# Kernel tuning notes

Measured on AMD Instinct MI355X. Metric: run time of the kernel, lower is better.

## Reference

```python
import jax, jax.numpy as jnp
import numpy as np

EPS = 1e-12

def _l2norm(x):
    n = jnp.sqrt(jnp.sum(x * x, axis=-1, keepdims=True))
    return x / jnp.maximum(n, EPS)

def setup_inputs() -> dict:
    key = jax.random.key(0)
    k1, k2 = jax.random.split(key)
    B, S, H = 32, 256, 768
    return {
        "query_embs": jax.random.normal(k1, (B, S, H), dtype=jnp.float32),
        "key_embs": jax.random.normal(k2, (B, S, H), dtype=jnp.float32),
        "q_mask": jnp.ones((B, S), dtype=jnp.float32),
        "k_mask": jnp.ones((B, S), dtype=jnp.float32),
        "alpha_raw": jnp.asarray(1.0, dtype=jnp.float32),
        "logit_scale": jnp.asarray(0.0, dtype=jnp.float32),  # log(1.0)
    }

def reference(query_embs, key_embs, q_mask, k_mask, alpha_raw, logit_scale):
    # query_embs, key_embs: (B, S, H); masks: (B, S)
    S = query_embs.shape[1]
    q = _l2norm(query_embs)
    k = _l2norm(key_embs)
    # all-pairs token similarity: (B, B, S, T)
    sim = jnp.einsum('ish,jth->ijst', q, k)
    # distance-decay weighting (do_distance=True, exp_decay=True)
    alpha = jax.nn.softplus(alpha_raw)
    pos = jnp.arange(S, dtype=jnp.float32)
    dist = jnp.abs(pos[:, None] - pos[None, :])  # (S, S)
    sim = sim * jnp.exp(-alpha * dist)
    # validity mask: (B, B, S, T)
    valid = (q_mask[:, None, :, None] * k_mask[None, :, None, :]) > 0
    scale = jnp.exp(logit_scale)
    neg_inf = jnp.float32(-jnp.inf)
    logits = jnp.where(valid, scale * sim, neg_inf)
    all_inf = jnp.all(logits == neg_inf, axis=-1, keepdims=True)
    safe_logits = jnp.where(all_inf, 0.0, logits)
    p = jax.nn.softmax(safe_logits, axis=-1)
    p = jnp.where(all_inf, 0.0, p)
    # softmax-weighted key aggregation: (B, B, S, H)
    agg = jnp.einsum('ijst,jth->ijsh', p, k)
    # per-token cosine score, masked mean over query tokens
    scores = jnp.einsum('ish,ijsh->ijs', q, agg) * q_mask[:, None, :]
    denom = jnp.clip(jnp.sum(q_mask, axis=-1, keepdims=True), 1.0, None)
    return jnp.sum(scores, axis=-1) / denom  # (B, B)
```

## Files before the change

kernel.cpp:

```cpp
#include <hip/hip_runtime.h>
#include <cmath>

#define BB 32
#define SS 256
#define HH 768

typedef __attribute__((ext_vector_type(8))) short bfrag8;
typedef __attribute__((ext_vector_type(4))) float accf4;

__device__ __forceinline__ unsigned short f2bf(float x) {
    unsigned int b = __float_as_uint(x);
    return (unsigned short)((b + 0x7FFFu + ((b >> 16) & 1u)) >> 16);
}

__device__ __forceinline__ float bf2f(unsigned short u) {
    unsigned int b = ((unsigned int)u) << 16;
    return __uint_as_float(b);
}


__global__ __launch_bounds__(256)
void normcvt_kernel(const float* __restrict__ Q, const float* __restrict__ K,
                    unsigned short* __restrict__ qws, unsigned short* __restrict__ kws) {
    const int wave = threadIdx.x >> 6, lane = threadIdx.x & 63;
    const bool isQ = blockIdx.x < 2048;
    const int rr = (blockIdx.x * 4 + wave) & 8191;
    const float4* src4 = isQ ? (const float4*)(Q + (size_t)rr * HH)
                             : (const float4*)(K + (size_t)rr * HH);
    float4 vv[3]; float s = 0.f;
#pragma unroll
    for (int c = 0; c < 3; ++c) {
        vv[c] = src4[lane + 64 * c];
        s += vv[c].x * vv[c].x + vv[c].y * vv[c].y + vv[c].z * vv[c].z + vv[c].w * vv[c].w;
    }
#pragma unroll
    for (int off = 1; off < 64; off <<= 1) s += __shfl_xor(s, off);
    float inv = 1.f / fmaxf(sqrtf(s), 1e-12f);

    const int b = rr >> 8, srow = rr & 255;
    unsigned short* dst = isQ ? qws : kws;
    const int fp8 = (lane & 7) * 4;
#pragma unroll
    for (int c = 0; c < 3; ++c) {
        int kc = (lane >> 3) + 8 * c;
        ushort4 o;
        o.x = f2bf(vv[c].x * inv); o.y = f2bf(vv[c].y * inv);
        o.z = f2bf(vv[c].z * inv); o.w = f2bf(vv[c].w * inv);
        *(ushort4*)(dst + (((size_t)b * 24 + kc) * 256 + srow) * 32 + fp8) = o;
    }
}

__global__ __launch_bounds__(256)
void ksum_kernel(const unsigned short* __restrict__ kws, const float* __restrict__ kmask,
                 unsigned short* __restrict__ ksumB) {
    __shared__ float red[8][32];
    const int j = blockIdx.x / 24, kc = blockIdx.x - j * 24;
    const int e = threadIdx.x & 31, tg = threadIdx.x >> 5;
    const unsigned short* base = kws + ((size_t)(j * 24 + kc)) * 8192;
    const float* km = kmask + j * SS;
    float s = 0.f;
    for (int t = tg; t < 256; t += 8) {
        if (km[t] > 0.f) s += bf2f(base[t * 32 + e]);
    }
    red[tg][e] = s;
    __syncthreads();
    if (tg == 0) {
        float tot = 0.f;
#pragma unroll
        for (int g = 0; g < 8; ++g) tot += red[g][e];
        ksumB[(size_t)(j * 24 + kc) * 32 + e] = f2bf(tot);
    }
}

__global__ __launch_bounds__(256, 3)
void mfma_kernel(const unsigned short* __restrict__ qws, const unsigned short* __restrict__ kws,
                 const float* __restrict__ qmask, const float* __restrict__ kmask,
                 const float* __restrict__ araw_p, const float* __restrict__ lscale_p,
                 const unsigned short* __restrict__ ksumB, float* __restrict__ out) {
    __shared__ short lKsum[768];
    __shared__ float sKm[256];
    __shared__ float wtab[13];
    __shared__ float sRed[4][2];
    __shared__ float sPart[4];
    __shared__ float sKcnt, sQden;

    const int tid = threadIdx.x;
    const int lane = tid & 63, w = tid >> 6;
    const int quad = lane >> 4, col = lane & 15;
    const int i = blockIdx.x >> 5, j = blockIdx.x & 31;

    const float alpha = log1pf(__expf(araw_p[0]));
    const float scale = __expf(lscale_p[0]);

    float aq = qmask[i * SS + tid];
    float km = kmask[j * SS + tid];
    sKm[tid] = km;
    float c = (km > 0.f) ? 1.f : 0.f;
#pragma unroll
    for (int off = 1; off < 64; off <<= 1) { aq += __shfl_xor(aq, off); c += __shfl_xor(c, off); }
    if (lane == 0) { sRed[w][0] = aq; sRed[w][1] = c; }
    if (tid < 13) wtab[tid] = __expf(-alpha * (float)tid);
    if (tid < 192) ((ushort4*)lKsum)[tid] = ((const ushort4*)(ksumB + (size_t)j * HH))[tid];
    __syncthreads();
    if (tid == 0) {
        sQden = fmaxf(sRed[0][0] + sRed[1][0] + sRed[2][0] + sRed[3][0], 1.f);
        sKcnt = sRed[0][1] + sRed[1][1] + sRed[2][1] + sRed[3][1];
    }
    __syncthreads();

    accf4 acc[4][3];
    accf4 accB[4];
#pragma unroll
    for (int a = 0; a < 4; ++a) {
        accB[a] = (accf4)0.f;
#pragma unroll
        for (int b = 0; b < 3; ++b) acc[a][b] = (accf4)0.f;
    }

    const unsigned short* qp0 = qws + (size_t)i * 24 * 8192 + (size_t)(4 * w) * 512
                                    + col * 32 + quad * 8;
    const unsigned short* kp0 = kws + (size_t)j * 24 * 8192 + col * 32 + quad * 8;

    for (int kc = 0; kc < 24; ++kc) {
        const unsigned short* qp = qp0 + (size_t)kc * 8192;
        const unsigned short* kp = kp0 + (size_t)kc * 8192;
        bfrag8 af[4];
#pragma unroll
        for (int sbl = 0; sbl < 4; ++sbl)
            af[sbl] = *(const bfrag8*)(qp + sbl * 512);
        bfrag8 bfr[6];
#pragma unroll
        for (int u = 0; u < 6; ++u) {
            int tb = 4 * w - 1 + u;
            if (tb >= 0 && tb <= 15)
                bfr[u] = *(const bfrag8*)(kp + tb * 512);
        }
        const bfrag8 kfrag = *(const bfrag8*)(lKsum + kc * 32 + quad * 8);
#pragma unroll
        for (int sbl = 0; sbl < 4; ++sbl) {
            accB[sbl] = __builtin_amdgcn_mfma_f32_16x16x32_bf16(af[sbl], kfrag, accB[sbl], 0, 0, 0);
#pragma unroll
            for (int dtb = 0; dtb < 3; ++dtb) {
                int tb = 4 * w + sbl - 1 + dtb;
                if (tb >= 0 && tb <= 15)
                    acc[sbl][dtb] = __builtin_amdgcn_mfma_f32_16x16x32_bf16(
                        af[sbl], bfr[sbl + dtb], acc[sbl][dtb], 0, 0, 0);
            }
        }
    }

    const float kcnt = sKcnt;
    float part = 0.f;
#pragma unroll
    for (int sbl = 0; sbl < 4; ++sbl) {
        const int sbase = (4 * w + sbl) * 16 + quad * 4;
        float ns[4] = {0.f, 0.f, 0.f, 0.f}, ds[4] = {0.f, 0.f, 0.f, 0.f};
#pragma unroll
        for (int dtb = 0; dtb < 3; ++dtb) {
            int tb = 4 * w + sbl - 1 + dtb;
            if (tb < 0 || tb > 15) continue;
            int t = tb * 16 + col;
            float kmv = sKm[t];
#pragma unroll
            for (int reg = 0; reg < 4; ++reg) {
                int st = sbase + reg;
                int d = t - st;
                bool ok = (d >= -11) && (d <= 12) && (kmv > 0.f);
                int idx = d < 0 ? -d : d;
                idx = ok ? idx : 0;
                float raw = acc[sbl][dtb][reg];
                float e = ok ? expm1f(scale * raw * wtab[idx]) : 0.f;
                ns[reg] = fmaf(e, raw, ns[reg]);
                ds[reg] += e;
            }
        }
#pragma unroll
        for (int off = 1; off < 16; off <<= 1) {
#pragma unroll
            for (int reg = 0; reg < 4; ++reg) {
                ns[reg] += __shfl_xor(ns[reg], off);
                ds[reg] += __shfl_xor(ds[reg], off);
            }
        }
        if (col == 0) {
#pragma unroll
            for (int reg = 0; reg < 4; ++reg) {
                int st = sbase + reg;
                float qm = qmask[i * SS + st];
                float bse = accB[sbl][reg];
                float dtot = ds[reg] + kcnt;
                float v = (qm > 0.f && kcnt > 0.f) ? qm * (ns[reg] + bse) / dtot : 0.f;
                part += v;
            }
        }
    }
    part += __shfl_xor(part, 16);
    part += __shfl_xor(part, 32);
    if (lane == 0) sPart[w] = part;
    __syncthreads();
    if (tid == 0) out[i * BB + j] = (sPart[0] + sPart[1] + sPart[2] + sPart[3]) / sQden;
}


extern "C" void kernel_launch(void* const* d_in, const int* in_sizes, int n_in,
                              void* d_out, int out_size, void* d_ws, size_t ws_size,
                              hipStream_t stream) {
    const float* Q      = (const float*)d_in[0];
    const float* K      = (const float*)d_in[1];
    const float* qmask  = (const float*)d_in[2];
    const float* kmask  = (const float*)d_in[3];
    const float* araw   = (const float*)d_in[4];
    const float* lscale = (const float*)d_in[5];
    float* outp = (float*)d_out;

    unsigned short* ksumB = (unsigned short*)d_ws;
    unsigned short* qws = ksumB + 24576;
    unsigned short* kws = qws + 6291456;

    normcvt_kernel<<<4096, 256, 0, stream>>>(Q, K, qws, kws);
    ksum_kernel<<<768, 256, 0, stream>>>(kws, kmask, ksumB);
    mfma_kernel<<<1024, 256, 0, stream>>>(qws, kws, qmask, kmask, araw, lscale, ksumB, outp);
}
```

Measured before the change: 175.8 us.

## Stage K tiles into LDS with double-buffered async global_load_lds and swizzle

The MFMA kernel now copies each 256x32 bf16 K chunk into shared memory using async global-to-LDS loads. It uses two buffers so the next chunk loads while the current one is computed. Before, every wave read its overlapping K fragments straight from global memory. The K workspace layout is XOR-swizzled in normcvt so the LDS fragment reads avoid bank conflicts, and ksum_kernel is rewritten to read that swizzled layout with vectorised loads. Occupancy is raised to 4 blocks per SM, which adds about 33KB of LDS per block and extra barriers per iteration.

Result: slower. 272.5 us (+55.0%).

```diff
diff --git a/kernel.cpp b/kernel.cpp
--- a/kernel.cpp
+++ b/kernel.cpp
@@ -16,6 +16,11 @@
 __device__ __forceinline__ float bf2f(unsigned short u) {
     unsigned int b = ((unsigned int)u) << 16;
     return __uint_as_float(b);
+}
+
+__device__ __forceinline__ void gload16(const void* g, void* l) {
+    __builtin_amdgcn_global_load_lds((const __attribute__((address_space(1))) void*)g,
+                                     (__attribute__((address_space(3))) void*)l, 16, 0, 0);
 }
 
 
@@ -39,7 +44,9 @@
 
     const int b = rr >> 8, srow = rr & 255;
     unsigned short* dst = isQ ? qws : kws;
-    const int fp8 = (lane & 7) * 4;
+    const int e = (lane & 7) * 4;
+    const int fp8 = isQ ? e
+                        : ((((e >> 3) ^ ((srow >> 1) & 3)) << 3) + (e & 7));
 #pragma unroll
     for (int c = 0; c < 3; ++c) {
         int kc = (lane >> 3) + 8 * c;
@@ -53,30 +60,46 @@
 __global__ __launch_bounds__(256)
 void ksum_kernel(const unsigned short* __restrict__ kws, const float* __restrict__ kmask,
                  unsigned short* __restrict__ ksumB) {
-    __shared__ float red[8][32];
+    __shared__ float red[4][8][4];
     const int j = blockIdx.x / 24, kc = blockIdx.x - j * 24;
-    const int e = threadIdx.x & 31, tg = threadIdx.x >> 5;
+    const int lane = threadIdx.x & 63, wv = threadIdx.x >> 6;
+    const int tg = threadIdx.x >> 3;
+    const int ec = threadIdx.x & 7;
     const unsigned short* base = kws + ((size_t)(j * 24 + kc)) * 8192;
     const float* km = kmask + j * SS;
-    float s = 0.f;
-    for (int t = tg; t < 256; t += 8) {
-        if (km[t] > 0.f) s += bf2f(base[t * 32 + e]);
-    }
-    red[tg][e] = s;
+    const int f = ec >> 1, off4 = (ec & 1) * 4;
+    float s0 = 0.f, s1 = 0.f, s2 = 0.f, s3 = 0.f;
+    for (int t = tg; t < 256; t += 32) {
+        if (km[t] > 0.f) {
+            int pos = ((f ^ ((t >> 1) & 3)) << 3) + off4;
+            ushort4 v = *(const ushort4*)(base + t * 32 + pos);
+            s0 += bf2f(v.x); s1 += bf2f(v.y); s2 += bf2f(v.z); s3 += bf2f(v.w);
+        }
+    }
+#pragma unroll
+    for (int off = 8; off < 64; off <<= 1) {
+        s0 += __shfl_xor(s0, off); s1 += __shfl_xor(s1, off);
+        s2 += __shfl_xor(s2, off); s3 += __shfl_xor(s3, off);
+    }
+    if ((lane >> 3) == 0) {
+        red[wv][ec][0] = s0; red[wv][ec][1] = s1; red[wv][ec][2] = s2; red[wv][ec][3] = s3;
+    }
     __syncthreads();
-    if (tg == 0) {
-        float tot = 0.f;
-#pragma unroll
-        for (int g = 0; g < 8; ++g) tot += red[g][e];
+    if (threadIdx.x < 32) {
+        int e = threadIdx.x;
+        float tot = red[0][e >> 2][e & 3] + red[1][e >> 2][e & 3]
+                  + red[2][e >> 2][e & 3] + red[3][e >> 2][e & 3];
         ksumB[(size_t)(j * 24 + kc) * 32 + e] = f2bf(tot);
     }
 }
 
-__global__ __launch_bounds__(256, 3)
+__global__ __launch_bounds__(256, 4)
 void mfma_kernel(const unsigned short* __restrict__ qws, const unsigned short* __restrict__ kws,
                  const float* __restrict__ qmask, const float* __restrict__ kmask,
                  const float* __restrict__ araw_p, const float* __restrict__ lscale_p,
                  const unsigned short* __restrict__ ksumB, float* __restrict__ out) {
+    __shared__ short lk0[8192];
+    __shared__ short lk1[8192];
     __shared__ short lKsum[768];
     __shared__ float sKm[256];
     __shared__ float wtab[13];
@@ -101,53 +124,71 @@
     if (lane == 0) { sRed[w][0] = aq; sRed[w][1] = c; }
     if (tid < 13) wtab[tid] = __expf(-alpha * (float)tid);
     if (tid < 192) ((ushort4*)lKsum)[tid] = ((const ushort4*)(ksumB + (size_t)j * HH))[tid];
+
+    accf4 acc[4][3];
+    accf4 accB[4];
+#pragma unroll
+    for (int a = 0; a < 4; ++a) {
+        accB[a] = (accf4)0.f;
+#pragma unroll
+        for (int b = 0; b < 3; ++b) acc[a][b] = (accf4)0.f;
+    }
+
+    const unsigned short* qp0 = qws + (size_t)i * 24 * 8192 + (size_t)(4 * w) * 512
+                                    + col * 32 + quad * 8;
+    const unsigned short* ksrc = kws + (size_t)j * 24 * 8192 + (size_t)w * 2048 + lane * 8;
+    const int perm8 = ((quad ^ ((col >> 1) & 3)) << 3);
+
+#define STAGEK(BUF, KCN) { \
+    unsigned short* _d = (unsigned short*)(BUF) + w * 2048; \
+    const unsigned short* _s = ksrc + (size_t)(KCN) * 8192; \
+    gload16(_s, _d); gload16(_s + 512, _d + 512); \
+    gload16(_s + 1024, _d + 1024); gload16(_s + 1536, _d + 1536); }
+
+#define COMPUTE(BUF, KC) { \
+    const unsigned short* _qp = qp0 + (size_t)(KC) * 8192; \
+    bfrag8 af[4]; \
+    af[0] = *(const bfrag8*)(_qp); \
+    af[1] = *(const bfrag8*)(_qp + 512); \
+    af[2] = *(const bfrag8*)(_qp + 1024); \
+    af[3] = *(const bfrag8*)(_qp + 1536); \
+    bfrag8 bfr[6]; \
+    _Pragma("unroll") \
+    for (int u = 0; u < 6; ++u) { \
+        int tb = 4 * w - 1 + u; \
+        if (tb >= 0 && tb <= 15) \
+            bfr[u] = *(const bfrag8*)((const short*)(BUF) + (size_t)(tb * 16 + col) * 32 + perm8); \
+    } \
+    const bfrag8 kfrag = *(const bfrag8*)(lKsum + (KC) * 32 + quad * 8); \
+    _Pragma("unroll") \
+    for (int sbl = 0; sbl < 4; ++sbl) { \
+        accB[sbl] = __builtin_amdgcn_mfma_f32_16x16x32_bf16(af[sbl], kfrag, accB[sbl], 0, 0, 0); \
+        _Pragma("unroll") \
+        for (int dtb = 0; dtb < 3; ++dtb) { \
+            int tb = 4 * w + sbl - 1 + dtb; \
+            if (tb >= 0 && tb <= 15) \
+                acc[sbl][dtb] = __builtin_amdgcn_mfma_f32_16x16x32_bf16( \
+                    af[sbl], bfr[sbl + dtb], acc[sbl][dtb], 0, 0, 0); \
+        } \
+    } }
+
+    STAGEK(lk0, 0);
     __syncthreads();
     if (tid == 0) {
         sQden = fmaxf(sRed[0][0] + sRed[1][0] + sRed[2][0] + sRed[3][0], 1.f);
         sKcnt = sRed[0][1] + sRed[1][1] + sRed[2][1] + sRed[3][1];
     }
-    __syncthreads();
-
-    accf4 acc[4][3];
-    accf4 accB[4];
-#pragma unroll
-    for (int a = 0; a < 4; ++a) {
-        accB[a] = (accf4)0.f;
-#pragma unroll
-        for (int b = 0; b < 3; ++b) acc[a][b] = (accf4)0.f;
-    }
-
-    const unsigned short* qp0 = qws + (size_t)i * 24 * 8192 + (size_t)(4 * w) * 512
-                                    + col * 32 + quad * 8;
-    const unsigned short* kp0 = kws + (size_t)j * 24 * 8192 + col * 32 + quad * 8;
-
-    for (int kc = 0; kc < 24; ++kc) {
-        const unsigned short* qp = qp0 + (size_t)kc * 8192;
-        const unsigned short* kp = kp0 + (size_t)kc * 8192;
-        bfrag8 af[4];
-#pragma unroll
-        for (int sbl = 0; sbl < 4; ++sbl)
-            af[sbl] = *(const bfrag8*)(qp + sbl * 512);
-        bfrag8 bfr[6];
-#pragma unroll
-        for (int u = 0; u < 6; ++u) {
-            int tb = 4 * w - 1 + u;
-            if (tb >= 0 && tb <= 15)
-                bfr[u] = *(const bfrag8*)(kp + tb * 512);
-        }
-        const bfrag8 kfrag = *(const bfrag8*)(lKsum + kc * 32 + quad * 8);
-#pragma unroll
-        for (int sbl = 0; sbl < 4; ++sbl) {
-            accB[sbl] = __builtin_amdgcn_mfma_f32_16x16x32_bf16(af[sbl], kfrag, accB[sbl], 0, 0, 0);
-#pragma unroll
-            for (int dtb = 0; dtb < 3; ++dtb) {
-                int tb = 4 * w + sbl - 1 + dtb;
-                if (tb >= 0 && tb <= 15)
-                    acc[sbl][dtb] = __builtin_amdgcn_mfma_f32_16x16x32_bf16(
-                        af[sbl], bfr[sbl + dtb], acc[sbl][dtb], 0, 0, 0);
-            }
-        }
-    }
+
+    for (int kc = 0; kc < 24; kc += 2) {
+        STAGEK(lk1, kc + 1);
+        COMPUTE(lk0, kc);
+        __syncthreads();
+        if (kc + 2 < 24) STAGEK(lk0, kc + 2);
+        COMPUTE(lk1, kc + 1);
+        __syncthreads();
+    }
+#undef STAGEK
+#undef COMPUTE
 
     const float kcnt = sKcnt;
     float part = 0.f;
```

## Stage K chunks into swizzled LDS via global_load_lds in MFMA kernel

Applied to the files above, without the earlier changes.

The MFMA kernel now copies each 256x32 K chunk into shared memory with direct global-to-LDS loads, then reads B fragments from LDS instead of global memory. Each K row is XOR-swizzled in the workspace layout to avoid LDS bank conflicts, and ksum is rewritten to read the swizzled layout with vectorized loads and shuffle reductions. Occupancy hint goes from 3 to 4 blocks. The goal is to stop each wave re-fetching overlapping K tiles from global memory; the cost is two block barriers per K step and 16KB more LDS per block.

New measurement: 153.8 us. -12.5%, faster.

```diff
diff --git a/kernel.cpp b/kernel.cpp
--- a/kernel.cpp
+++ b/kernel.cpp
@@ -14,8 +14,12 @@
 }
 
 __device__ __forceinline__ float bf2f(unsigned short u) {
-    unsigned int b = ((unsigned int)u) << 16;
-    return __uint_as_float(b);
+    return __uint_as_float(((unsigned int)u) << 16);
+}
+
+__device__ __forceinline__ void gload16(const void* g, void* l) {
+    __builtin_amdgcn_global_load_lds((const __attribute__((address_space(1))) void*)g,
+                                     (__attribute__((address_space(3))) void*)l, 16, 0, 0);
 }
 
 
@@ -39,7 +43,9 @@
 
     const int b = rr >> 8, srow = rr & 255;
     unsigned short* dst = isQ ? qws : kws;
-    const int fp8 = (lane & 7) * 4;
+    const int e = (lane & 7) * 4;
+    const int fp8 = isQ ? e
+                        : ((((e >> 3) ^ ((srow >> 1) & 3)) << 3) + (e & 7));
 #pragma unroll
     for (int c = 0; c < 3; ++c) {
         int kc = (lane >> 3) + 8 * c;
@@ -53,30 +59,45 @@
 __global__ __launch_bounds__(256)
 void ksum_kernel(const unsigned short* __restrict__ kws, const float* __restrict__ kmask,
                  unsigned short* __restrict__ ksumB) {
-    __shared__ float red[8][32];
+    __shared__ float red[4][8][4];
     const int j = blockIdx.x / 24, kc = blockIdx.x - j * 24;
-    const int e = threadIdx.x & 31, tg = threadIdx.x >> 5;
+    const int lane = threadIdx.x & 63, wv = threadIdx.x >> 6;
+    const int tg = threadIdx.x >> 3;
+    const int ec = threadIdx.x & 7;
     const unsigned short* base = kws + ((size_t)(j * 24 + kc)) * 8192;
     const float* km = kmask + j * SS;
-    float s = 0.f;
-    for (int t = tg; t < 256; t += 8) {
-        if (km[t] > 0.f) s += bf2f(base[t * 32 + e]);
-    }
-    red[tg][e] = s;
-    __syncthreads();
-    if (tg == 0) {
-        float tot = 0.f;
-#pragma unroll
-        for (int g = 0; g < 8; ++g) tot += red[g][e];
-        ksumB[(size_t)(j * 24 + kc) * 32 + e] = f2bf(tot);
-    }
-}
-
-__global__ __launch_bounds__(256, 3)
+    const int f = ec >> 1, off4 = (ec & 1) * 4;
+    float s0 = 0.f, s1 = 0.f, s2 = 0.f, s3 = 0.f;
+    for (int t = tg; t < 256; t += 32) {
+        if (km[t] > 0.f) {
+            int pos = ((f ^ ((t >> 1) & 3)) << 3) + off4;
+            ushort4 v = *(const ushort4*)(base + t * 32 + pos);
+            s0 += bf2f(v.x); s1 += bf2f(v.y); s2 += bf2f(v.z); s3 += bf2f(v.w);
+        }
+    }
+#pragma unroll
+    for (int off = 8; off < 64; off <<= 1) {
+        s0 += __shfl_xor(s0, off); s1 += __shfl_xor(s1, off);
+        s2 += __shfl_xor(s2, off); s3 += __shfl_xor(s3, off);
+    }
+    if ((lane >> 3) == 0) {
+        red[wv][ec][0] = s0; red[wv][ec][1] = s1; red[wv][ec][2] = s2; red[wv][ec][3] = s3;
+    }
+    __syncthreads();
+    if (threadIdx.x < 32) {
+        int e2 = threadIdx.x;
+        float tot = red[0][e2 >> 2][e2 & 3] + red[1][e2 >> 2][e2 & 3]
+                  + red[2][e2 >> 2][e2 & 3] + red[3][e2 >> 2][e2 & 3];
+        ksumB[(size_t)(j * 24 + kc) * 32 + e2] = f2bf(tot);
+    }
+}
+
+__global__ __launch_bounds__(256, 4)
 void mfma_kernel(const unsigned short* __restrict__ qws, const unsigned short* __restrict__ kws,
                  const float* __restrict__ qmask, const float* __restrict__ kmask,
                  const float* __restrict__ araw_p, const float* __restrict__ lscale_p,
                  const unsigned short* __restrict__ ksumB, float* __restrict__ out) {
+    __shared__ __align__(16) short lk[8192];
     __shared__ short lKsum[768];
     __shared__ float sKm[256];
     __shared__ float wtab[13];
@@ -106,7 +127,6 @@
         sQden = fmaxf(sRed[0][0] + sRed[1][0] + sRed[2][0] + sRed[3][0], 1.f);
         sKcnt = sRed[0][1] + sRed[1][1] + sRed[2][1] + sRed[3][1];
     }
-    __syncthreads();
 
     accf4 acc[4][3];
     accf4 accB[4];
@@ -119,23 +139,34 @@
 
     const unsigned short* qp0 = qws + (size_t)i * 24 * 8192 + (size_t)(4 * w) * 512
                                     + col * 32 + quad * 8;
-    const unsigned short* kp0 = kws + (size_t)j * 24 * 8192 + col * 32 + quad * 8;
+    const size_t kb0 = (size_t)j * 24 * 8192;
+    const int perm8 = ((quad ^ ((col >> 1) & 3)) << 3);
 
     for (int kc = 0; kc < 24; ++kc) {
+        __syncthreads();
+        {
+            const unsigned short* ks = kws + kb0 + (size_t)kc * 8192 + w * 2048 + lane * 8;
+            unsigned short* lkd = (unsigned short*)lk + w * 2048;
+#pragma unroll
+            for (int n = 0; n < 4; ++n)
+                gload16(ks + n * 512, lkd + n * 512);
+        }
+        __syncthreads();
+
         const unsigned short* qp = qp0 + (size_t)kc * 8192;
-        const unsigned short* kp = kp0 + (size_t)kc * 8192;
         bfrag8 af[4];
 #pragma unroll
         for (int sbl = 0; sbl < 4; ++sbl)
             af[sbl] = *(const bfrag8*)(qp + sbl * 512);
+
+        const bfrag8 kfrag = *(const bfrag8*)(lKsum + kc * 32 + quad * 8);
         bfrag8 bfr[6];
 #pragma unroll
         for (int u = 0; u < 6; ++u) {
             int tb = 4 * w - 1 + u;
             if (tb >= 0 && tb <= 15)
-                bfr[u] = *(const bfrag8*)(kp + tb * 512);
-        }
-        const bfrag8 kfrag = *(const bfrag8*)(lKsum + kc * 32 + quad * 8);
+                bfr[u] = *(const bfrag8*)(lk + (size_t)(tb * 16 + col) * 32 + perm8);
+        }
 #pragma unroll
         for (int sbl = 0; sbl < 4; ++sbl) {
             accB[sbl] = __builtin_amdgcn_mfma_f32_16x16x32_bf16(af[sbl], kfrag, accB[sbl], 0, 0, 0);
@@ -149,6 +180,7 @@
         }
     }
 
+    __syncthreads();
     const float kcnt = sKcnt;
     float part = 0.f;
 #pragma unroll
```
